# Kernel tuning notes

Hardware: AMD Instinct MI355X
Metric: run time of the kernel (lower is better)

## Reference

```python
import jax, jax.numpy as jnp
import numpy as np

B, N = 32, 128
V, P, L = 50000, 40, 50
WD, UD = 100, 25
D = WD + UD          # 125: LSTM hidden per direction
H2 = 2 * D           # 250: BiLSTM output
HID = 100            # hidden_dim for scorers


def setup_inputs() -> dict:
    key = jax.random.key(0)
    ks = iter(jax.random.split(key, 40))
    p = lambda shape: jax.random.normal(next(ks), shape, jnp.float32) * 0.05
    inp = {
        'word_ids': jax.random.randint(next(ks), (B, N), 0, V),
        'upos_ids': jax.random.randint(next(ks), (B, N), 0, P),
        'target_arcs': jax.random.randint(next(ks), (B, N), 0, N),
        'wlookup': p((V, WD)),
        'tlookup': p((V, UD)),  # original sizes tag table by word_count
        # LSTM layer 0 (input D=125), layer 1 (input 2D=250); f=fwd, b=bwd dir
        'l0f_Wih': p((4 * D, D)), 'l0f_Whh': p((4 * D, D)), 'l0f_b': p((4 * D,)),
        'l0b_Wih': p((4 * D, D)), 'l0b_Whh': p((4 * D, D)), 'l0b_b': p((4 * D,)),
        'l1f_Wih': p((4 * D, H2)), 'l1f_Whh': p((4 * D, D)), 'l1f_b': p((4 * D,)),
        'l1b_Wih': p((4 * D, H2)), 'l1b_Whh': p((4 * D, D)), 'l1b_b': p((4 * D,)),
        'eh_W': p((HID, H2)), 'eh_b': p((HID,)),
        'em_W': p((HID, H2)), 'em_b': p((HID,)),
        'es_W': p((1, HID)), 'es_b': p((1,)),
        'lh_W': p((HID, H2)), 'lh_b': p((HID,)),
        'lm_W': p((HID, H2)), 'lm_b': p((HID,)),
        'ls_W': p((L, HID)), 'ls_b': p((L,)),
    }
    return inp


def _lstm_dir(x, Wih, Whh, b, reverse):
    # x: [B,T,in] -> h: [B,T,H], pytorch gate order i,f,g,o
    H = Whh.shape[1]
    xg = jnp.einsum('bti,gi->btg', x, Wih) + b  # precompute input projections

    def step(carry, xt):
        h, c = carry
        g = xt + h @ Whh.T
        i, f, gg, o = jnp.split(g, 4, axis=-1)
        c = jax.nn.sigmoid(f) * c + jax.nn.sigmoid(i) * jnp.tanh(gg)
        h = jax.nn.sigmoid(o) * jnp.tanh(c)
        return (h, c), h

    h0 = jnp.zeros((x.shape[0], H), x.dtype)
    _, hs = jax.lax.scan(step, (h0, h0), jnp.swapaxes(xg, 0, 1), reverse=reverse)
    return jnp.swapaxes(hs, 0, 1)


def _bilstm(x, Wf, Uf, bf, Wb, Ub, bb):
    return jnp.concatenate([_lstm_dir(x, Wf, Uf, bf, False),
                            _lstm_dir(x, Wb, Ub, bb, True)], axis=-1)


def reference(word_ids, upos_ids, target_arcs, wlookup, tlookup,
              l0f_Wih, l0f_Whh, l0f_b, l0b_Wih, l0b_Whh, l0b_b,
              l1f_Wih, l1f_Whh, l1f_b, l1b_Wih, l1b_Whh, l1b_b,
              eh_W, eh_b, em_W, em_b, es_W, es_b,
              lh_W, lh_b, lm_W, lm_b, ls_W, ls_b):
    n = word_ids.shape[1]
    words = jnp.concatenate([wlookup[word_ids], tlookup[upos_ids]], axis=-1)  # [B,N,125]
    h0 = _bilstm(words, l0f_Wih, l0f_Whh, l0f_b, l0b_Wih, l0b_Whh, l0b_b)
    word_exprs = _bilstm(h0, l1f_Wih, l1f_Whh, l1f_b, l1b_Wih, l1b_Whh, l1b_b)  # [B,N,250]

    word_h = word_exprs @ eh_W.T + eh_b  # [B,N,100]
    word_m = word_exprs @ em_W.T + em_b
    # fused pairwise biaffine-style scoring (replaces the O(n) python loop)
    pair = jnp.tanh(word_h[:, :, None, :] + word_m[:, None, :, :])  # [B,N,N,100]
    arc_scores = jnp.einsum('bijh,h->bij', pair, es_W[0]) + es_b[0]  # [B,N,N]

    # training path: margin augmentation
    target_arcs = target_arcs.at[:, 0].set(0)
    margin = 1.0 - jax.nn.one_hot(target_arcs, n, dtype=arc_scores.dtype)
    arc_scores = arc_scores + margin

    # decode() is an external MST decoder; greedy argmax stand-in
    parsed_trees = jnp.argmax(arc_scores, axis=-1)

    tree = target_arcs  # is_train path
    rel_heads = jnp.take_along_axis(word_exprs, tree[:, :, None], axis=1)  # [B,N,250]
    rel_heads = rel_heads @ lh_W.T + lh_b
    rel_mod = word_exprs @ lm_W.T + lm_b
    rel_scores = jnp.tanh(rel_mod + rel_heads) @ ls_W.T + ls_b  # [B,N,L]
    predicted_rels = jnp.argmax(rel_scores, axis=-1)
    return (parsed_trees, predicted_rels, arc_scores, rel_scores)
```

## Files before the change

### kernel.cpp

```cpp
#include <hip/hip_runtime.h>
#include <hip/hip_bf16.h>
#include <hip/hip_fp16.h>
#include <math.h>

#define B 32
#define N 128
#define BT (B*N)
#define WD 100
#define UD 25
#define D 125
#define G4 (4*D)
#define H2 (2*D)
#define HID 100
#define L 50

__device__ __forceinline__ float fast_tanh(float x) {
    float e = __expf(2.0f * x);
    return 1.0f - 2.0f / (e + 1.0f);
}
__device__ __forceinline__ float fast_sigmoid(float x) {
    return 1.0f / (1.0f + __expf(-x));
}
__device__ __forceinline__ float bcast_lane(float v, int k) {
    return __builtin_bit_cast(float, __builtin_amdgcn_readlane(__builtin_bit_cast(int, v), k));
}
__device__ __forceinline__ unsigned bcast_lane_u(unsigned v, int k) {
    return (unsigned)__builtin_amdgcn_readlane((int)v, k);
}

__device__ __forceinline__ unsigned pack_f16x2(float lo, float hi) {
    __half hl = __float2half_rn(lo), hh = __float2half_rn(hi);
    unsigned a = (unsigned)__builtin_bit_cast(unsigned short, hl);
    unsigned b = (unsigned)__builtin_bit_cast(unsigned short, hh);
    return a | (b << 16);
}

typedef _Float16 h2_t __attribute__((ext_vector_type(2)));
__device__ __forceinline__ float dot2acc(unsigned wu, unsigned hu, float acc) {
#if __has_builtin(__builtin_amdgcn_fdot2)
    return __builtin_amdgcn_fdot2(__builtin_bit_cast(h2_t, wu),
                                  __builtin_bit_cast(h2_t, hu), acc, false);
#else
    h2_t wv = __builtin_bit_cast(h2_t, wu);
    h2_t hv = __builtin_bit_cast(h2_t, hu);
    acc = fmaf((float)wv[0], (float)hv[0], acc);
    acc = fmaf((float)wv[1], (float)hv[1], acc);
    return acc;
#endif
}

struct TJob { const float* src; float* dst; int R, C, ldo, coff, tile0, tiles_x; };
struct TArgs { TJob j[8]; };

__global__ __launch_bounds__(256)
void setup_fused(TArgs a, int n_tr,
                 const int* __restrict__ wids, const int* __restrict__ uids,
                 const float* __restrict__ wl, const float* __restrict__ tl,
                 float* __restrict__ words,
                 const float* __restrict__ l0f_b, const float* __restrict__ l0b_b,
                 const float* __restrict__ l1f_b, const float* __restrict__ l1b_b,
                 const float* __restrict__ eh_b, const float* __restrict__ em_b,
                 const float* __restrict__ lm_b,
                 float* __restrict__ b_l0, float* __restrict__ b_l1,
                 float* __restrict__ b_s3,
                 const float* __restrict__ s0, const float* __restrict__ s1,
                 const float* __restrict__ s2, const float* __restrict__ s3w,
                 unsigned* __restrict__ d0, unsigned* __restrict__ d1,
                 unsigned* __restrict__ d2, unsigned* __restrict__ d3) {
    __shared__ float tile[32][33];
    int bid = blockIdx.x;
    int tid = threadIdx.x;
    if (bid < n_tr) {
        int ji = 0;
        #pragma unroll
        for (int i = 1; i < 8; i++) if (bid >= a.j[i].tile0) ji = i;
        TJob jb = a.j[ji];
        int t = bid - jb.tile0;
        int tx = t % jb.tiles_x, ty = t / jb.tiles_x;
        int txx = tid & 31, tyy = tid >> 5;
        int k0 = tx*32, n0 = ty*32;
        #pragma unroll
        for (int dy = 0; dy < 32; dy += 8) {
            int n = n0 + tyy + dy, k = k0 + txx;
            if (n < jb.R && k < jb.C)
                tile[tyy+dy][txx] = jb.src[(size_t)n*jb.C + k];
        }
        __syncthreads();
        #pragma unroll
        for (int dy = 0; dy < 32; dy += 8) {
            int k = k0 + tyy + dy, n = n0 + txx;
            if (k < jb.C && n < jb.R)
                jb.dst[(size_t)k*jb.ldo + jb.coff + n] = tile[txx][tyy+dy];
        }
        return;
    }
    bid -= n_tr;
    if (bid < 2048) {
        int bt = bid*2 + (tid >> 7);
        int t = tid & 127;
        int wid = wids[bt], uid = uids[bt];
        if (t < WD)       words[bt*D + t] = wl[(size_t)wid*WD + t];
        else if (t < D)   words[bt*D + t] = tl[(size_t)uid*UD + (t - WD)];
        return;
    }
    bid -= 2048;
    if (bid < 9) {
        int t = bid*256 + tid;
        if (t < 500)        b_l0[t] = l0f_b[t];
        else if (t < 1000)  b_l0[t] = l0b_b[t-500];
        else if (t < 1500)  b_l1[t-1000] = l1f_b[t-1000];
        else if (t < 2000)  b_l1[t-1000] = l1b_b[t-1500];
        else if (t < 2100)  b_s3[t-2000] = eh_b[t-2000];
        else if (t < 2200)  b_s3[t-2000] = em_b[t-2100];
        else if (t < 2300)  b_s3[t-2000] = lm_b[t-2200];
        return;
    }
    bid -= 9;
    int e = bid*256 + tid;
    int m = e >> 15;
    int r = e & 32767;
    int pk = r >> 9;
    int g  = r & 511;
    const float* s = (m == 0) ? s0 : (m == 1) ? s1 : (m == 2) ? s2 : s3w;
    unsigned* dd   = (m == 0) ? d0 : (m == 1) ? d1 : (m == 2) ? d2 : d3;
    float v0 = 0.0f, v1 = 0.0f;
    if (g < 500) {
        int k0 = pk << 1;
        if (k0 < 125)     v0 = s[(size_t)g*125 + k0];
        if (k0 + 1 < 125) v1 = s[(size_t)g*125 + k0 + 1];
    }
    dd[(pk << 9) + g] = pack_f16x2(v0, v1);
}

#define MT 16
template<int CPT, int BD>
__device__ __forceinline__
void proj_body(const float* __restrict__ x, const float* __restrict__ WT,
               const float* __restrict__ bias, float* __restrict__ out,
               int Ncols, int K, int ldx, const int* __restrict__ gather_idx,
               int blk, float* xs) {
    int m0 = blk * MT;
    for (int e = threadIdx.x; e < MT * K; e += BD) {
        int r = e / K, k = e - r * K;
        int m = m0 + r;
        int row = m;
        if (gather_idx) {
            int bb = m >> 7, np = m & 127;
            row = (bb << 7) + (np == 0 ? 0 : gather_idx[m]);
        }
        xs[k*17 + r] = x[(size_t)row*ldx + k];
    }
    __syncthreads();
    int n0 = threadIdx.x;
    int lane = threadIdx.x & 63;
    float acc[CPT][MT];
    int ncl[CPT];
    #pragma unroll
    for (int j = 0; j < CPT; j++) {
        int n = n0 + j*BD;
        ncl[j] = (n < Ncols) ? n : (Ncols - 1);
        #pragma unroll
        for (int r = 0; r < MT; r++) acc[j][r] = 0.0f;
    }
    float wkc[4][CPT];
    #pragma unroll
    for (int q = 0; q < 4; q++)
        #pragma unroll
        for (int j = 0; j < CPT; j++)
            wkc[q][j] = WT[(size_t)q*Ncols + ncl[j]];
    int k0 = 0;
    for (; k0 + 8 <= K; k0 += 4) {
        float xv = xs[(k0 + (lane >> 4))*17 + (lane & 15)];
        float wkn[4][CPT];
        #pragma unroll
        for (int q = 0; q < 4; q++)
            #pragma unroll
            for (int j = 0; j < CPT; j++)
                wkn[q][j] = WT[(size_t)(k0 + 4 + q)*Ncols + ncl[j]];
        #pragma unroll
        for (int q = 0; q < 4; q++) {
            #pragma unroll
            for (int r = 0; r < 16; r++) {
                float hv = bcast_lane(xv, q*16 + r);
                #pragma unroll
                for (int j = 0; j < CPT; j++)
                    acc[j][r] = fmaf(wkc[q][j], hv, acc[j][r]);
            }
        }
        #pragma unroll
        for (int q = 0; q < 4; q++)
            #pragma unroll
            for (int j = 0; j < CPT; j++)
                wkc[q][j] = wkn[q][j];
    }
    {
        float xv = xs[(k0 + (lane >> 4))*17 + (lane & 15)];
        #pragma unroll
        for (int q = 0; q < 4; q++) {
            #pragma unroll
            for (int r = 0; r < 16; r++) {
                float hv = bcast_lane(xv, q*16 + r);
                #pragma unroll
                for (int j = 0; j < CPT; j++)
                    acc[j][r] = fmaf(wkc[q][j], hv, acc[j][r]);
            }
        }
        k0 += 4;
    }
    for (; k0 < K; k0++) {
        float xv = xs[k0*17 + (lane & 15)];
        float wk[CPT];
        #pragma unroll
        for (int j = 0; j < CPT; j++) wk[j] = WT[(size_t)k0*Ncols + ncl[j]];
        #pragma unroll
        for (int r = 0; r < 16; r++) {
            float hv = bcast_lane(xv, r);
            #pragma unroll
            for (int j = 0; j < CPT; j++)
                acc[j][r] = fmaf(wk[j], hv, acc[j][r]);
        }
    }
    #pragma unroll
    for (int j = 0; j < CPT; j++) {
        int n = n0 + j*BD;
        if (n < Ncols) {
            float bb = bias[n];
            #pragma unroll
            for (int r = 0; r < MT; r++) out[(size_t)(m0 + r)*Ncols + n] = acc[j][r] + bb;
        }
    }
}

__global__ __launch_bounds__(512)
void proj_t(const float* __restrict__ x, const float* __restrict__ WT,
            const float* __restrict__ bias, float* __restrict__ out,
            int Ncols, int K, int ldx) {
    __shared__ float xs[250 * 17 + 16];
    proj_body<2, 512>(x, WT, bias, out, Ncols, K, ldx, nullptr, blockIdx.x, xs);
}

__global__ __launch_bounds__(256)
void proj_s3lh(const float* __restrict__ x,
               const float* __restrict__ WTa, const float* __restrict__ ba,
               float* __restrict__ outa,
               const float* __restrict__ WTb, const float* __restrict__ bb,
               float* __restrict__ outb, const int* __restrict__ gather_idx) {
    __shared__ float xs[250 * 17 + 16];
    int job = blockIdx.x >> 8;
    int blk = blockIdx.x & 255;
    if (job == 0)
        proj_body<2, 256>(x, WTa, ba, outa, 300, H2, H2, nullptr, blk, xs);
    else
        proj_body<2, 256>(x, WTb, bb, outb, 100, H2, H2, gather_idx, blk, xs);
}

__global__ __launch_bounds__(512, 2)
void lstm_scan(const float* __restrict__ xgc,
               const unsigned* __restrict__ WhHf, const unsigned* __restrict__ WhHb,
               float* __restrict__ out) {
    int dir = blockIdx.x & 1;
    int b = blockIdx.x >> 1;
    const unsigned* WhH = dir ? WhHb : WhHf;
    int off = dir ? D : 0;
    int t = threadIdx.x;
    int lane = t & 63;
    int w = t >> 6;
    int ks = w >> 1;
    int cg = ((w & 1) << 6) + lane;
    int c0 = cg << 2;

    __shared__ __align__(16) float hbuf[128];
    __shared__ __align__(16) float pbuf[4*512];

    const unsigned* wp = WhH + (size_t)(ks*16)*512 + c0;

    const float* xb = xgc + (size_t)b * N * 1000 + dir * 500;
    bool xa = (ks == 0) && (cg < 125);
    float4 zero4 = make_float4(0.f, 0.f, 0.f, 0.f);
    float4 xA = zero4, xB = zero4;
    if (xa) {
        xA = *(const float4*)&xb[(size_t)(dir ? (N-1) : 0)*1000 + c0];
        xB = *(const float4*)&xb[(size_t)(dir ? (N-2) : 1)*1000 + c0];
    }

    if (t < 128) hbuf[t] = 0.0f;
    __syncthreads();

    float c = 0.0f;
    for (int ti = 0; ti < N; ti++) {
        int tt = dir ? (N-1-ti) : ti;
        uint4 wq[16];
        #pragma unroll
        for (int p = 0; p < 16; p++)
            wq[p] = *(const uint4*)&wp[(size_t)p*512];
        float2 h2 = *(const float2*)&hbuf[ks*32 + ((lane & 15) << 1)];
        unsigned vhp = pack_f16x2(h2.x, h2.y);
        float4 x_cur = xA;
        float4 xC = zero4;
        if (xa && ti + 2 < N) {
            int tn = dir ? (tt-2) : (tt+2);
            xC = *(const float4*)&xb[(size_t)tn*1000 + c0];
        }
        float a0 = x_cur.x, a1 = x_cur.y, a2 = x_cur.z, a3 = x_cur.w;
        #pragma unroll
        for (int p = 0; p < 16; p++) {
            unsigned hp = bcast_lane_u(vhp, p);
            a0 = dot2acc(wq[p].x, hp, a0);
            a1 = dot2acc(wq[p].y, hp, a1);
            a2 = dot2acc(wq[p].z, hp, a2);
            a3 = dot2acc(wq[p].w, hp, a3);
        }
        xA = xB; xB = xC;
        *(float4*)&pbuf[ks*512 + c0] = make_float4(a0, a1, a2, a3);
        asm volatile("s_waitcnt lgkmcnt(0)" ::: "memory");
        __builtin_amdgcn_s_barrier();
        asm volatile("" ::: "memory");
        if (t < D) {
            float iv = pbuf[t]       + pbuf[512+t]       + pbuf[1024+t]       + pbuf[1536+t];
            float fv = pbuf[125+t]   + pbuf[512+125+t]   + pbuf[1024+125+t]   + pbuf[1536+125+t];
            float gv = pbuf[250+t]   + pbuf[512+250+t]   + pbuf[1024+250+t]   + pbuf[1536+250+t];
            float ov = pbuf[375+t]   + pbuf[512+375+t]   + pbuf[1024+375+t]   + pbuf[1536+375+t];
            float si = fast_sigmoid(iv);
            float sf = fast_sigmoid(fv);
            float so = fast_sigmoid(ov);
            c = sf * c + si * fast_tanh(gv);
            float h = so * fast_tanh(c);
            hbuf[t] = h;
            out[(size_t)(b*N + tt)*H2 + off + t] = h;
        }
        asm volatile("s_waitcnt lgkmcnt(0)" ::: "memory");
        __builtin_amdgcn_s_barrier();
        asm volatile("" ::: "memory");
    }
}

#define ITILE 8
__global__ __launch_bounds__(128)
void arc_score(const float* __restrict__ s3,
               const float* __restrict__ esW, const float* __restrict__ esb,
               const int* __restrict__ ta,
               float* __restrict__ arc_out, float* __restrict__ tree_out) {
    __shared__ float wms[128 * 101];
    __shared__ float whs[ITILE][HID];
    __shared__ float es[HID];
    __shared__ float sv[128];
    __shared__ int   si[128];
    int j = threadIdx.x;
    int blk = blockIdx.x;
    int b = blk >> 4, it = blk & 15;

    for (int e = j; e < 128 * 25; e += 128) {
        int r = e / 25, cc = e - r * 25;
        float4 v = *(const float4*)&s3[(size_t)(b*N + r)*300 + 100 + (cc << 2)];
        float* dst = &wms[r*101 + (cc << 2)];
        dst[0] = v.x; dst[1] = v.y; dst[2] = v.z; dst[3] = v.w;
    }
    for (int e = j; e < ITILE * 25; e += 128) {
        int ii = e / 25, cc = e - ii * 25;
        float4 v = *(const float4*)&s3[(size_t)(b*N + it*ITILE + ii)*300 + (cc << 2)];
        float* dst = &whs[ii][cc << 2];
        dst[0] = v.x; dst[1] = v.y; dst[2] = v.z; dst[3] = v.w;
    }
    if (j < HID) es[j] = esW[j];
    __syncthreads();
    float eb = esb[0];
    const float* wmr = &wms[j * 101];
    float acc[ITILE];
    #pragma unroll
    for (int ii = 0; ii < ITILE; ii++) acc[ii] = 0.0f;
    for (int h = 0; h < HID; h++) {
        float wm = wmr[h];
        float ev = es[h];
        #pragma unroll
        for (int ii = 0; ii < ITILE; ii++)
            acc[ii] = fmaf(ev, fast_tanh(whs[ii][h] + wm), acc[ii]);
    }
    for (int ii = 0; ii < ITILE; ii++) {
        int i = it * ITILE + ii;
        int bi = b * N + i;
        int tai = (i == 0) ? 0 : ta[bi];
        float score = acc[ii] + eb + 1.0f - ((j == tai) ? 1.0f : 0.0f);
        arc_out[(size_t)bi*N + j] = score;
        sv[j] = score; si[j] = j;
        __syncthreads();
        for (int s = 64; s; s >>= 1) {
            if (j < s) {
                float ov = sv[j+s]; int oi = si[j+s];
                if (ov > sv[j] || (ov == sv[j] && oi < si[j])) { sv[j] = ov; si[j] = oi; }
            }
            __syncthreads();
        }
        if (j == 0) tree_out[bi] = (float)si[0];
        __syncthreads();
    }
}

__global__ __launch_bounds__(128)
void rel_score(const float* __restrict__ s3, const float* __restrict__ rh,
               const float* __restrict__ lsW, const float* __restrict__ lsb,
               float* __restrict__ rel_out, float* __restrict__ pred_out) {
    __shared__ float tv[HID];
    __shared__ float sv[128];
    __shared__ int   si[128];
    int bt = blockIdx.x;
    int j = threadIdx.x;
    if (j < HID)
        tv[j] = fast_tanh(s3[(size_t)bt*300 + 200 + j] + rh[(size_t)bt*HID + j]);
    __syncthreads();
    float score = -1e30f;
    if (j < L) {
        float acc = 0.0f;
        const float* wrow = lsW + j*HID;
        for (int h = 0; h < HID; h++) acc = fmaf(wrow[h], tv[h], acc);
        score = acc + lsb[j];
        rel_out[(size_t)bt*L + j] = score;
    }
    sv[j] = score; si[j] = j;
    __syncthreads();
    for (int s = 64; s; s >>= 1) {
        if (j < s) {
            float ov = sv[j+s]; int oi = si[j+s];
            if (ov > sv[j] || (ov == sv[j] && oi < si[j])) { sv[j] = ov; si[j] = oi; }
        }
        __syncthreads();
    }
    if (j == 0) pred_out[bt] = (float)si[0];
}

extern "C" void kernel_launch(void* const* d_in, const int* in_sizes, int n_in,
                              void* d_out, int out_size, void* d_ws, size_t ws_size,
                              hipStream_t stream) {
    const int*   word_ids    = (const int*)  d_in[0];
    const int*   upos_ids    = (const int*)  d_in[1];
    const int*   target_arcs = (const int*)  d_in[2];
    const float* wlookup     = (const float*)d_in[3];
    const float* tlookup     = (const float*)d_in[4];
    const float* l0f_Wih = (const float*)d_in[5];
    const float* l0f_Whh = (const float*)d_in[6];
    const float* l0f_b   = (const float*)d_in[7];
    const float* l0b_Wih = (const float*)d_in[8];
    const float* l0b_Whh = (const float*)d_in[9];
    const float* l0b_b   = (const float*)d_in[10];
    const float* l1f_Wih = (const float*)d_in[11];
    const float* l1f_Whh = (const float*)d_in[12];
    const float* l1f_b   = (const float*)d_in[13];
    const float* l1b_Wih = (const float*)d_in[14];
    const float* l1b_Whh = (const float*)d_in[15];
    const float* l1b_b   = (const float*)d_in[16];
    const float* eh_W = (const float*)d_in[17];
    const float* eh_b = (const float*)d_in[18];
    const float* em_W = (const float*)d_in[19];
    const float* em_b = (const float*)d_in[20];
    const float* es_W = (const float*)d_in[21];
    const float* es_b = (const float*)d_in[22];
    const float* lh_W = (const float*)d_in[23];
    const float* lh_b = (const float*)d_in[24];
    const float* lm_W = (const float*)d_in[25];
    const float* lm_b = (const float*)d_in[26];
    const float* ls_W = (const float*)d_in[27];
    const float* ls_b = (const float*)d_in[28];

    float* out = (float*)d_out;
    float* trees_out = out;
    float* preds_out = out + BT;
    float* arc_out   = out + 2*BT;
    float* rel_out   = out + 2*BT + BT*N;

    float* ws = (float*)d_ws;
    float* A       = ws;
    float* words   = ws + 4096000;
    float* C       = ws + 4608000;
    float* WT_l0   = ws + 5632000;
    float* WT_l1   = ws + 5757000;
    float* WT_s3   = ws + 6007000;
    float* WT_lh   = ws + 6082000;
    unsigned* WhH_l0f = (unsigned*)(ws + 6107000);
    unsigned* WhH_l0b = (unsigned*)(ws + 6139768);
    unsigned* WhH_l1f = (unsigned*)(ws + 6172536);
    unsigned* WhH_l1b = (unsigned*)(ws + 6205304);
    float* b_l0    = ws + 6238072;
    float* b_l1    = ws + 6239072;
    float* b_s3    = ws + 6240072;
    float* rel_head = ws + 6241072;

    TArgs ta{};
    int n_tr = 0;
    {
        auto tiles = [](int R, int C_) { return ((C_+31)/32) * ((R+31)/32); };
        struct { const float* s; float* d; int R, C, ldo, coff; } js[8] = {
            { l0f_Wih, WT_l0, 500, 125, 1000, 0 },
            { l0b_Wih, WT_l0, 500, 125, 1000, 500 },
            { l1f_Wih, WT_l1, 500, 250, 1000, 0 },
            { l1b_Wih, WT_l1, 500, 250, 1000, 500 },
            { eh_W, WT_s3, 100, 250, 300, 0 },
            { em_W, WT_s3, 100, 250, 300, 100 },
            { lm_W, WT_s3, 100, 250, 300, 200 },
            { lh_W, WT_lh, 100, 250, 100, 0 },
        };
        for (int i = 0; i < 8; i++) {
            ta.j[i].src = js[i].s;  ta.j[i].dst = js[i].d;
            ta.j[i].R = js[i].R;    ta.j[i].C = js[i].C;
            ta.j[i].ldo = js[i].ldo; ta.j[i].coff = js[i].coff;
            ta.j[i].tile0 = n_tr;
            ta.j[i].tiles_x = (js[i].C + 31) / 32;
            n_tr += tiles(js[i].R, js[i].C);
        }
    }
    setup_fused<<<n_tr + 2048 + 9 + 512, 256, 0, stream>>>(
        ta, n_tr, word_ids, upos_ids, wlookup, tlookup, words,
        l0f_b, l0b_b, l1f_b, l1b_b, eh_b, em_b, lm_b,
        b_l0, b_l1, b_s3,
        l0f_Whh, l0b_Whh, l1f_Whh, l1b_Whh,
        WhH_l0f, WhH_l0b, WhH_l1f, WhH_l1b);

    proj_t<<<BT/MT, 512, 0, stream>>>(words, WT_l0, b_l0, A, 1000, D, D);

    lstm_scan<<<B*2, 512, 0, stream>>>(A, WhH_l0f, WhH_l0b, C);

    proj_t<<<BT/MT, 512, 0, stream>>>(C, WT_l1, b_l1, A, 1000, H2, H2);

    lstm_scan<<<B*2, 512, 0, stream>>>(A, WhH_l1f, WhH_l1b, C);

    proj_s3lh<<<512, 256, 0, stream>>>(C, WT_s3, b_s3, A,
                                       WT_lh, lh_b, rel_head, target_arcs);

    arc_score<<<512, 128, 0, stream>>>(A, es_W, es_b, target_arcs,
                                       arc_out, trees_out);

    rel_score<<<BT, 128, 0, stream>>>(A, rel_head, ls_W, ls_b,
                                      rel_out, preds_out);
}
```

Baseline: 508.4 us.

## Compute LSTM cell redundantly per wave to drop second barrier per step

Each wave now computes the LSTM cell update for the 32 hidden units it consumes, rather than having one set of threads write h to shared memory, and the other waves pick up h through a lane shuffle in registers. The partial-sum buffer is double-buffered by step parity, which removes the second block-wide barrier and the hbuf round trip from the recurrence. The cost is duplicated gate math across the two waves sharing a k-slice, plus extra shared-memory reads of partials. Only one wave per pair writes the output.

```diff
diff --git a/kernel.cpp b/kernel.cpp
--- a/kernel.cpp
+++ b/kernel.cpp
@@ -258,6 +258,7 @@
 void lstm_scan(const float* __restrict__ xgc,
                const unsigned* __restrict__ WhHf, const unsigned* __restrict__ WhHb,
                float* __restrict__ out) {
+    __shared__ __align__(16) float pbuf[2][4*512];
     int dir = blockIdx.x & 1;
     int b = blockIdx.x >> 1;
     const unsigned* WhH = dir ? WhHb : WhHf;
@@ -269,9 +270,6 @@
     int cg = ((w & 1) << 6) + lane;
     int c0 = cg << 2;
 
-    __shared__ __align__(16) float hbuf[128];
-    __shared__ __align__(16) float pbuf[4*512];
-
     const unsigned* wp = WhH + (size_t)(ks*16)*512 + c0;
 
     const float* xb = xgc + (size_t)b * N * 1000 + dir * 500;
@@ -283,18 +281,19 @@
         xB = *(const float4*)&xb[(size_t)(dir ? (N-2) : 1)*1000 + c0];
     }
 
-    if (t < 128) hbuf[t] = 0.0f;
-    __syncthreads();
-
-    float c = 0.0f;
+    int t4 = ks*32 + (lane & 31);
+    bool act = (lane < 32) && (t4 < 125);
+    bool sto = act && ((w & 1) == 0);
+
+    unsigned vhp = 0;
+    float c = 0.0f, h = 0.0f;
+
     for (int ti = 0; ti < N; ti++) {
         int tt = dir ? (N-1-ti) : ti;
         uint4 wq[16];
         #pragma unroll
         for (int p = 0; p < 16; p++)
             wq[p] = *(const uint4*)&wp[(size_t)p*512];
-        float2 h2 = *(const float2*)&hbuf[ks*32 + ((lane & 15) << 1)];
-        unsigned vhp = pack_f16x2(h2.x, h2.y);
         float4 x_cur = xA;
         float4 xC = zero4;
         if (xa && ti + 2 < N) {
@@ -304,33 +303,33 @@
         float a0 = x_cur.x, a1 = x_cur.y, a2 = x_cur.z, a3 = x_cur.w;
         #pragma unroll
         for (int p = 0; p < 16; p++) {
-            unsigned hp = bcast_lane_u(vhp, p);
+            unsigned hp = bcast_lane_u(vhp, 2*p);
             a0 = dot2acc(wq[p].x, hp, a0);
             a1 = dot2acc(wq[p].y, hp, a1);
             a2 = dot2acc(wq[p].z, hp, a2);
             a3 = dot2acc(wq[p].w, hp, a3);
         }
         xA = xB; xB = xC;
-        *(float4*)&pbuf[ks*512 + c0] = make_float4(a0, a1, a2, a3);
+        float* pb = &pbuf[ti & 1][0];
+        *(float4*)&pb[ks*512 + c0] = make_float4(a0, a1, a2, a3);
         asm volatile("s_waitcnt lgkmcnt(0)" ::: "memory");
         __builtin_amdgcn_s_barrier();
         asm volatile("" ::: "memory");
-        if (t < D) {
-            float iv = pbuf[t]       + pbuf[512+t]       + pbuf[1024+t]       + pbuf[1536+t];
-            float fv = pbuf[125+t]   + pbuf[512+125+t]   + pbuf[1024+125+t]   + pbuf[1536+125+t];
-            float gv = pbuf[250+t]   + pbuf[512+250+t]   + pbuf[1024+250+t]   + pbuf[1536+250+t];
-            float ov = pbuf[375+t]   + pbuf[512+375+t]   + pbuf[1024+375+t]   + pbuf[1536+375+t];
+        if (act) {
+            float iv = pb[t4]       + pb[512+t4]       + pb[1024+t4]       + pb[1536+t4];
+            float fv = pb[125+t4]   + pb[512+125+t4]   + pb[1024+125+t4]   + pb[1536+125+t4];
+            float gv = pb[250+t4]   + pb[512+250+t4]   + pb[1024+250+t4]   + pb[1536+250+t4];
+            float ov = pb[375+t4]   + pb[512+375+t4]   + pb[1024+375+t4]   + pb[1536+375+t4];
             float si = fast_sigmoid(iv);
             float sf = fast_sigmoid(fv);
             float so = fast_sigmoid(ov);
             c = sf * c + si * fast_tanh(gv);
-            float h = so * fast_tanh(c);
-            hbuf[t] = h;
-            out[(size_t)(b*N + tt)*H2 + off + t] = h;
-        }
-        asm volatile("s_waitcnt lgkmcnt(0)" ::: "memory");
-        __builtin_amdgcn_s_barrier();
-        asm volatile("" ::: "memory");
+            h = so * fast_tanh(c);
+            if (sto)
+                out[(size_t)(b*N + tt)*H2 + off + t4] = h;
+        }
+        float hn = __shfl_xor(h, 1);
+        vhp = pack_f16x2(h, hn);
     }
 }
 
```

Result: slower. 551.1 us (+8.4%).
